# Kernel tuning notes

Measured on AMD Instinct MI355X. Metric: run time of the kernel, lower is better.

The kernel has to match this reference:

```python
import jax, jax.numpy as jnp
import numpy as np

N = 4096
INPUT_DIM = 512
H1 = 256
H2 = 64
ALPHA = 0.2
MASK_VAL = -9e15


def setup_inputs() -> dict:
    key = jax.random.key(0)
    ks = jax.random.split(key, 10)

    def glorot(k, fan_in, fan_out):
        r = np.sqrt(6.0 / (fan_in + fan_out)).astype(np.float32)
        return jax.random.uniform(k, (fan_in, fan_out), jnp.float32, -r, r)

    return {
        "X": jax.random.normal(ks[0], (N, INPUT_DIM), jnp.float32),
        "adj": jax.random.randint(ks[1], (N, N), 0, 2, jnp.int32),
        "noise": jax.random.normal(ks[2], (N, H2), jnp.float32),
        "W0": glorot(ks[3], INPUT_DIM, H1),
        "a0": jax.random.normal(ks[4], (2 * H1, 1), jnp.float32) * 0.1,
        "W1": glorot(ks[5], H1, H2),
        "a1": jax.random.normal(ks[6], (2 * H2, 1), jnp.float32) * 0.1,
        "W2": glorot(ks[7], H1, H2),
        "a2": jax.random.normal(ks[8], (2 * H2, 1), jnp.float32) * 0.1,
    }


def gat_layer(X, W, a, adj):
    # h: [N, d]
    h = X @ W
    d = h.shape[1]
    # e_ij = leakyrelu(a^T [h_i ; h_j]) == leakyrelu(f1_i + f2_j)
    f1 = h @ a[:d]            # [N, 1]
    f2 = h @ a[d:]            # [N, 1]
    e = jax.nn.leaky_relu(f1 + f2.T, negative_slope=ALPHA)  # [N, N]
    e = jnp.where(adj > 0, e, MASK_VAL)
    attn = jax.nn.softmax(e, axis=1)  # dropout omitted (eval mode)
    return attn @ h


def reference(X, adj, noise, W0, a0, W1, a1, W2, a2):
    hidden = gat_layer(X, W0, a0, adj)
    mean = gat_layer(hidden, W1, a1, adj)
    logstd = gat_layer(hidden, W2, a2, adj)
    Z = noise * jnp.exp(logstd) + mean          # [N, H2]
    A_pred = jax.nn.sigmoid(Z @ Z.T)            # [N, N]
    return A_pred
```

## Files before the change

### kernel.cpp

```cpp
#include <hip/hip_runtime.h>
#include <hip/hip_bf16.h>
#include <math.h>

#define N_NODES 4096
#define DIM_IN  512
#define DH1     256
#define DH2     64
#define ALPHA   0.2f
#define ROW_WORDS (N_NODES / 64)
#define NWORDS  (N_NODES * ROW_WORDS)
#define L2E     1.4426950408889634f

typedef __bf16 bf16_t;
typedef bf16_t bf16x8 __attribute__((ext_vector_type(8)));
typedef float  f32x4  __attribute__((ext_vector_type(4)));


__global__ __launch_bounds__(256) void prep_kernel(
    const float* __restrict__ X, const float* __restrict__ W0,
    const float* __restrict__ W1, const float* __restrict__ W2,
    const int* __restrict__ adj,
    bf16_t* __restrict__ Xb, bf16_t* __restrict__ W0T,
    bf16_t* __restrict__ W12T, unsigned long long* __restrict__ mask,
    float* __restrict__ f1b, float* __restrict__ f2b)
{
    const int b = blockIdx.x;
    const int tid = threadIdx.x;
    if (b < 2048) {
        int i = b * 256 + tid;
        float4 v = ((const float4*)X)[i];
        bf16_t o[4] = {(bf16_t)v.x, (bf16_t)v.y, (bf16_t)v.z, (bf16_t)v.w};
        const int e = i * 4;
        const int row = e >> 9, k = e & 511;
        const size_t base = ((size_t)(row >> 4) * 64 + (k >> 3)) * 128 + (row & 15) * 8 + (k & 7);
        *(uint2*)(Xb + base) = *(const uint2*)o;
    } else if (b < 2560) {
        int o = (b - 2048) * 256 + tid;
        int n = o >> 9, k = o & 511;
        const size_t base = ((size_t)(n >> 4) * 64 + (k >> 3)) * 128 + (n & 15) * 8 + (k & 7);
        W0T[base] = (bf16_t)W0[(size_t)k * DH1 + n];
    } else if (b < 2688) {
        int o = (b - 2560) * 256 + tid;
        int n = o >> 8, k = o & 255;
        const float* W = (n < 64) ? W1 : W2;
        const size_t base = ((size_t)(n >> 4) * 32 + (k >> 3)) * 128 + (n & 15) * 8 + (k & 7);
        W12T[base] = (bf16_t)W[(size_t)k * 64 + (n & 63)];
    } else if (b < 4736) {
        const int lane = tid & 63;
        int gw = ((b - 2688) * 256 + tid) >> 6;
        for (int w = gw; w < NWORDS; w += 8192) {
            int v = adj[(size_t)w * 64 + lane];
            unsigned long long bb = __ballot(v > 0);
            if (lane == 0) mask[w] = bb;
        }
    } else {
        int zb = b - 4736;
        float4* dst = (float4*)((zb < 8) ? f1b : f2b);
        dst[(zb & 7) * 256 + tid] = float4{0.f, 0.f, 0.f, 0.f};
    }
}

__global__ __launch_bounds__(256) void rowstats_kernel(
    const unsigned long long* __restrict__ mask,
    const float* __restrict__ f1b, const float* __restrict__ f2b,
    float* __restrict__ mrowb, float* __restrict__ srowb)
{
    __shared__ float f2s[N_NODES];
    const int l = blockIdx.y;
    const float* f1 = f1b + (size_t)l * N_NODES;
    const float* f2 = f2b + (size_t)l * N_NODES;
    const int tid = threadIdx.x;
    #pragma unroll
    for (int j = 0; j < N_NODES / 4; j += 256)
        ((float4*)f2s)[j + tid] = ((const float4*)f2)[j + tid];
    __syncthreads();
    const int wave = tid >> 6, lane = tid & 63;
    const int row = blockIdx.x * 4 + wave;
    const float fi = f1[row];
    const int l5 = lane & 31;
    const bool lohalf = (lane < 32);

    const unsigned long long wv = mask[(size_t)row * ROW_WORDS + lane];
    const unsigned wlo = (unsigned)wv, whi = (unsigned)(wv >> 32);

    float mx = -3.0e38f;
    #pragma unroll
    for (int t = 0; t < ROW_WORDS; ++t) {
        const unsigned blo = __shfl(wlo, t), bhi = __shfl(whi, t);
        const unsigned sel = lohalf ? blo : bhi;
        if ((sel >> l5) & 1u) {
            float e = fi + f2s[t * 64 + lane];
            e = fmaxf(e, ALPHA * e);
            mx = fmaxf(mx, e);
        }
    }
    for (int off = 32; off; off >>= 1) mx = fmaxf(mx, __shfl_xor(mx, off));

    float sum = 0.f;
    if (mx > -2.0e38f) {
        #pragma unroll
        for (int t = 0; t < ROW_WORDS; ++t) {
            const unsigned blo = __shfl(wlo, t), bhi = __shfl(whi, t);
            const unsigned sel = lohalf ? blo : bhi;
            if ((sel >> l5) & 1u) {
                float e = fi + f2s[t * 64 + lane];
                e = fmaxf(e, ALPHA * e);
                sum += __expf(e - mx);
            }
        }
    }
    for (int off = 32; off; off >>= 1) sum += __shfl_xor(sum, off);
    if (lane == 0) {
        if (mx > -2.0e38f) { mrowb[l * N_NODES + row] = mx; srowb[l * N_NODES + row] = sum; }
        else               { mrowb[l * N_NODES + row] = 0.f; srowb[l * N_NODES + row] = 0.f; }
    }
}

template <int NT, int KLEN>
__global__ __launch_bounds__(256) void attn_fused_kernel(
    const unsigned long long* __restrict__ maskw,
    const float* __restrict__ f1, const float* __restrict__ f2,
    const float* __restrict__ mrow, const float* __restrict__ srow,
    const bf16_t* __restrict__ BT, float* __restrict__ outP, int N)
{
    __shared__ float f2s[KLEN];
    __shared__ float tile[64 * (NT * 16 + 4)];
    const int tid = threadIdx.x;
    const int wave = tid >> 6, lane = tid & 63, quad = lane >> 4, l16 = lane & 15;
    const int colBase = blockIdx.x * (NT * 16);
    const int rowBase = blockIdx.y * 64;
    const int kBeg = blockIdx.z * KLEN;
    const int r = rowBase + wave * 16 + l16;

    if (tid < KLEN / 4) ((float4*)f2s)[tid] = *(const float4*)(f2 + kBeg + tid * 4);

    const float m = mrow[r], s = srow[r];
    const bool uni = (s <= 0.f);
    const float Cr = uni ? 0.f : (-m * L2E - __log2f(s));
    const float f1r = f1[r];
    const float puni = 1.0f / (float)N_NODES;

    __syncthreads();

    const int ubase = (colBase >> 4) * (N_NODES * 16) + kBeg * 16;
    const int laneo = quad * 128 + l16 * 8;
    const int qs = quad * 8;
    const unsigned long long* mptr = maskw + (size_t)r * ROW_WORDS + (kBeg >> 6);

    f32x4 acc[NT] = {};
    unsigned long long mcur = mptr[0];
    for (int w = 0; w < KLEN / 64; ++w) {
        unsigned long long mnext = (w < KLEN / 64 - 1) ? mptr[w + 1] : 0ull;
        const unsigned mlo = (unsigned)mcur, mhi = (unsigned)(mcur >> 32);
        #pragma unroll
        for (int h = 0; h < 2; ++h) {
            const int k0 = w * 64 + h * 32;
            bf16x8 bv[NT];
            #pragma unroll
            for (int t = 0; t < NT; ++t)
                bv[t] = *(const bf16x8*)(BT + ubase + t * (N_NODES * 16) + k0 * 16 + laneo);
            const unsigned bits = ((h ? mhi : mlo) >> qs) & 0xFFu;
            const int kc = k0 + qs;
            bf16x8 av;
            #pragma unroll
            for (int j = 0; j < 8; ++j) {
                float x = f1r + f2s[kc + j];
                float e = fmaxf(x, ALPHA * x);
                float p = ((bits >> j) & 1u) ? exp2f(__builtin_fmaf(e, L2E, Cr)) : 0.f;
                av[j] = (bf16_t)(uni ? puni : p);
            }
            #pragma unroll
            for (int t = 0; t < NT; ++t)
                acc[t] = __builtin_amdgcn_mfma_f32_16x16x32_bf16(av, bv[t], acc[t], 0, 0, 0);
        }
        mcur = mnext;
    }

    #pragma unroll
    for (int t = 0; t < NT; ++t) {
        const int col = t * 16 + l16;
        #pragma unroll
        for (int rr = 0; rr < 4; ++rr)
            tile[(wave * 16 + quad * 4 + rr) * (NT * 16 + 4) + col] = acc[t][rr];
    }
    __syncthreads();
    const int half = lane >> 5, c32 = (lane & 31) * 4;
    float* outBase = outP + (size_t)blockIdx.z * N_NODES * N + (size_t)rowBase * N + colBase;
    #pragma unroll
    for (int p = 0; p < 8; ++p) {
        const int rl = p * 8 + wave * 2 + half;
        f32x4 v = *(const f32x4*)&tile[rl * (NT * 16 + 4) + c32];
        __builtin_nontemporal_store(v, (f32x4*)(outBase + (size_t)rl * N + c32));
    }
}

template <int KLEN>
__global__ __launch_bounds__(256) void attn12_kernel(
    const unsigned long long* __restrict__ maskw,
    const float* __restrict__ f1b, const float* __restrict__ f2b,
    const float* __restrict__ mrowb, const float* __restrict__ srowb,
    const bf16_t* __restrict__ h12T, float* __restrict__ outP)
{
    __shared__ float f2s[KLEN];
    __shared__ float tile[64 * 68];
    const int l = blockIdx.x;
    const float* f1 = f1b + (size_t)l * N_NODES;
    const float* f2 = f2b + (size_t)l * N_NODES;

    const int tid = threadIdx.x;
    const int wave = tid >> 6, lane = tid & 63, quad = lane >> 4, l16 = lane & 15;
    const int rowBase = blockIdx.y * 64;
    const int kBeg = blockIdx.z * KLEN;
    const int r = rowBase + wave * 16 + l16;

    if (tid < KLEN / 4) ((float4*)f2s)[tid] = *(const float4*)(f2 + kBeg + tid * 4);

    const float m = mrowb[l * N_NODES + r], s = srowb[l * N_NODES + r];
    const bool uni = (s <= 0.f);
    const float Cr = uni ? 0.f : (-m * L2E - __log2f(s));
    const float f1r = f1[r];
    const float puni = 1.0f / (float)N_NODES;

    __syncthreads();

    const int ubase = (l * 4) * (N_NODES * 16) + kBeg * 16;
    const int laneo = quad * 128 + l16 * 8;
    const int qs = quad * 8;
    const unsigned long long* mptr = maskw + (size_t)r * ROW_WORDS + (kBeg >> 6);

    f32x4 acc[4] = {};
    unsigned long long mcur = mptr[0];
    for (int w = 0; w < KLEN / 64; ++w) {
        unsigned long long mnext = (w < KLEN / 64 - 1) ? mptr[w + 1] : 0ull;
        const unsigned mlo = (unsigned)mcur, mhi = (unsigned)(mcur >> 32);
        #pragma unroll
        for (int h = 0; h < 2; ++h) {
            const int k0 = w * 64 + h * 32;
            bf16x8 bv[4];
            #pragma unroll
            for (int t = 0; t < 4; ++t)
                bv[t] = *(const bf16x8*)(h12T + ubase + t * (N_NODES * 16) + k0 * 16 + laneo);
            const unsigned bits = ((h ? mhi : mlo) >> qs) & 0xFFu;
            const int kc = k0 + qs;
            bf16x8 av;
            #pragma unroll
            for (int j = 0; j < 8; ++j) {
                float x = f1r + f2s[kc + j];
                float e = fmaxf(x, ALPHA * x);
                float p = ((bits >> j) & 1u) ? exp2f(__builtin_fmaf(e, L2E, Cr)) : 0.f;
                av[j] = (bf16_t)(uni ? puni : p);
            }
            #pragma unroll
            for (int t = 0; t < 4; ++t)
                acc[t] = __builtin_amdgcn_mfma_f32_16x16x32_bf16(av, bv[t], acc[t], 0, 0, 0);
        }
        mcur = mnext;
    }

    #pragma unroll
    for (int t = 0; t < 4; ++t) {
        const int col = t * 16 + l16;
        #pragma unroll
        for (int rr = 0; rr < 4; ++rr)
            tile[(wave * 16 + quad * 4 + rr) * 68 + col] = acc[t][rr];
    }
    __syncthreads();
    const int q4 = lane >> 4, c16 = (lane & 15) * 4;
    float* outBase = outP + ((size_t)blockIdx.z * 2 + l) * (N_NODES * DH2) + (size_t)rowBase * DH2;
    #pragma unroll
    for (int p = 0; p < 4; ++p) {
        const int rl = p * 16 + wave * 4 + q4;
        f32x4 v = *(const f32x4*)&tile[rl * 68 + c16];
        __builtin_nontemporal_store(v, (f32x4*)(outBase + (size_t)rl * DH2 + c16));
    }
}

__global__ __launch_bounds__(256) void reduce_kernel(
    const float* __restrict__ p, bf16_t* __restrict__ out, int n4, int S)
{
    int i = blockIdx.x * 256 + threadIdx.x;
    if (i >= n4) return;
    float4 a = ((const float4*)p)[i];
    for (int s = 1; s < S; ++s) {
        float4 b = ((const float4*)p)[(size_t)s * n4 + i];
        a.x += b.x; a.y += b.y; a.z += b.z; a.w += b.w;
    }
    bf16_t o[4] = {(bf16_t)a.x, (bf16_t)a.y, (bf16_t)a.z, (bf16_t)a.w};
    const int e = i * 4;
    const int row = e >> 8, k = e & 255;
    const size_t base = ((size_t)(row >> 4) * 32 + (k >> 3)) * 128 + (row & 15) * 8 + (k & 7);
    *(uint2*)(out + base) = *(const uint2*)o;
}

__global__ __launch_bounds__(256) void reduce_z_kernel(
    const float* __restrict__ part, const float* __restrict__ noise,
    bf16_t* __restrict__ ZA, bf16_t* __restrict__ ZB)
{
    const int idx = blockIdx.x * 256 + threadIdx.x;
    const int stride = 2 * N_NODES * DH2;
    float mean = 0.f, ls = 0.f;
    #pragma unroll
    for (int s = 0; s < 4; ++s) {
        mean += part[(size_t)s * stride + idx];
        ls   += part[(size_t)s * stride + N_NODES * DH2 + idx];
    }
    float z = noise[idx] * __expf(ls) + mean;
    bf16_t zhi = (bf16_t)z;
    bf16_t zlo = (bf16_t)(z - (float)zhi);
    const int i = idx >> 6, c = idx & 63;
    const size_t base = ((size_t)(i >> 4) * 32 + (c >> 3)) * 128 + (i & 15) * 8 + (c & 7);
    ZA[base]        = zhi;
    ZA[base + 1024] = zhi;
    ZA[base + 2048] = zlo;
    ZA[base + 3072] = zlo;
    ZB[base]        = zhi;
    ZB[base + 1024] = zlo;
    ZB[base + 2048] = zhi;
    ZB[base + 3072] = zlo;
}

template <int NT>
__global__ __launch_bounds__(256) void gemm0_kernel(
    const bf16_t* __restrict__ A, const bf16_t* __restrict__ BT,
    bf16_t* __restrict__ Ct, const float* __restrict__ a0,
    float* __restrict__ f1, float* __restrict__ f2)
{
    const int tid = threadIdx.x;
    const int wave = tid >> 6, lane = tid & 63, quad = lane >> 4, l16 = lane & 15;
    const int colBase = blockIdx.x * (NT * 16), rowBase = blockIdx.y * 64;
    const size_t KS = (size_t)DIM_IN * 16;
    const bf16_t* Ap = A + (size_t)((rowBase >> 4) + wave) * KS + quad * 128 + l16 * 8;
    const bf16_t* Bp = BT + (size_t)(colBase >> 4) * KS + quad * 128 + l16 * 8;

    f32x4 acc[NT] = {};
    for (int k0 = 0; k0 < DIM_IN; k0 += 64) {
        bf16x8 bv[2 * NT];
        #pragma unroll
        for (int t = 0; t < NT; ++t) {
            bv[t]      = *(const bf16x8*)(Bp + (size_t)t * KS + k0 * 16);
            bv[NT + t] = *(const bf16x8*)(Bp + (size_t)t * KS + (k0 + 32) * 16);
        }
        bf16x8 av0 = *(const bf16x8*)(Ap + k0 * 16);
        bf16x8 av1 = *(const bf16x8*)(Ap + (k0 + 32) * 16);
        #pragma unroll
        for (int t = 0; t < NT; ++t)
            acc[t] = __builtin_amdgcn_mfma_f32_16x16x32_bf16(av0, bv[t], acc[t], 0, 0, 0);
        #pragma unroll
        for (int t = 0; t < NT; ++t)
            acc[t] = __builtin_amdgcn_mfma_f32_16x16x32_bf16(av1, bv[NT + t], acc[t], 0, 0, 0);
    }
    #pragma unroll
    for (int t = 0; t < NT; ++t) {
        const int col = colBase + t * 16 + l16;
        bf16_t pk[4];
        #pragma unroll
        for (int rr = 0; rr < 4; ++rr) pk[rr] = (bf16_t)acc[t][rr];
        const int kc = (rowBase + wave * 16 + quad * 4) >> 3;
        const size_t o = ((size_t)(col >> 4) * (N_NODES >> 3) + kc) * 128
                       + (col & 15) * 8 + (quad & 1) * 4;
        *(uint2*)(Ct + o) = *(const uint2*)pk;
    }
    #pragma unroll
    for (int rr = 0; rr < 4; ++rr) {
        float s1 = 0.f, s2 = 0.f;
        #pragma unroll
        for (int t = 0; t < NT; ++t) {
            const int col = colBase + t * 16 + l16;
            s1 += acc[t][rr] * a0[col];
            s2 += acc[t][rr] * a0[DH1 + col];
        }
        #pragma unroll
        for (int off = 8; off; off >>= 1) {
            s1 += __shfl_down(s1, off, 16);
            s2 += __shfl_down(s2, off, 16);
        }
        if (l16 == 0) {
            const int row = rowBase + wave * 16 + quad * 4 + rr;
            atomicAdd(f1 + row, s1);
            atomicAdd(f2 + row, s2);
        }
    }
}

__global__ __launch_bounds__(256) void gemm12_kernel(
    const bf16_t* __restrict__ A, const bf16_t* __restrict__ BT,
    bf16_t* __restrict__ Ct, const float* __restrict__ a1, const float* __restrict__ a2,
    float* __restrict__ f1b, float* __restrict__ f2b)
{
    const int tid = threadIdx.x;
    const int wave = tid >> 6, lane = tid & 63, quad = lane >> 4, l16 = lane & 15;
    const int l = blockIdx.x;
    const int colBase = l * 64, rowBase = blockIdx.y * 64;
    const size_t KS = (size_t)DH1 * 16;
    const bf16_t* Ap = A + (size_t)((rowBase >> 4) + wave) * KS + quad * 128 + l16 * 8;
    const bf16_t* Bp = BT + (size_t)(colBase >> 4) * KS + quad * 128 + l16 * 8;

    f32x4 acc[4] = {};
    for (int k0 = 0; k0 < DH1; k0 += 64) {
        bf16x8 bv[8];
        #pragma unroll
        for (int t = 0; t < 4; ++t) {
            bv[t]     = *(const bf16x8*)(Bp + (size_t)t * KS + k0 * 16);
            bv[4 + t] = *(const bf16x8*)(Bp + (size_t)t * KS + (k0 + 32) * 16);
        }
        bf16x8 av0 = *(const bf16x8*)(Ap + k0 * 16);
        bf16x8 av1 = *(const bf16x8*)(Ap + (k0 + 32) * 16);
        #pragma unroll
        for (int t = 0; t < 4; ++t)
            acc[t] = __builtin_amdgcn_mfma_f32_16x16x32_bf16(av0, bv[t], acc[t], 0, 0, 0);
        #pragma unroll
        for (int t = 0; t < 4; ++t)
            acc[t] = __builtin_amdgcn_mfma_f32_16x16x32_bf16(av1, bv[4 + t], acc[t], 0, 0, 0);
    }
    #pragma unroll
    for (int t = 0; t < 4; ++t) {
        const int col = colBase + t * 16 + l16;
        bf16_t pk[4];
        #pragma unroll
        for (int rr = 0; rr < 4; ++rr) pk[rr] = (bf16_t)acc[t][rr];
        const int kc = (rowBase + wave * 16 + quad * 4) >> 3;
        const size_t o = ((size_t)(col >> 4) * (N_NODES >> 3) + kc) * 128
                       + (col & 15) * 8 + (quad & 1) * 4;
        *(uint2*)(Ct + o) = *(const uint2*)pk;
    }
    const float* a = l ? a2 : a1;
    #pragma unroll
    for (int rr = 0; rr < 4; ++rr) {
        float s1 = 0.f, s2 = 0.f;
        #pragma unroll
        for (int t = 0; t < 4; ++t) {
            const int lc = t * 16 + l16;
            s1 += acc[t][rr] * a[lc];
            s2 += acc[t][rr] * a[64 + lc];
        }
        #pragma unroll
        for (int off = 8; off; off >>= 1) {
            s1 += __shfl_down(s1, off, 16);
            s2 += __shfl_down(s2, off, 16);
        }
        if (l16 == 0) {
            const int row = rowBase + wave * 16 + quad * 4 + rr;
            f1b[l * N_NODES + row] = s1;
            f2b[l * N_NODES + row] = s2;
        }
    }
}

template <int NT>
__global__ __launch_bounds__(256) void zzt_sigmoid_kernel(
    const bf16_t* __restrict__ ZA, const bf16_t* __restrict__ ZB, float* __restrict__ C)
{
    __shared__ float tile[64 * (NT * 16 + 4)];
    const int tid = threadIdx.x;
    const int wave = tid >> 6, lane = tid & 63, quad = lane >> 4, l16 = lane & 15;
    const int colBase = blockIdx.x * (NT * 16), rowBase = blockIdx.y * 64;
    const bf16_t* Ap = ZA + (size_t)((rowBase >> 4) + wave) * 4096 + quad * 128 + l16 * 8;
    const bf16_t* Bp = ZB + (size_t)(colBase >> 4) * 4096 + quad * 128 + l16 * 8;

    f32x4 acc[NT] = {};
    for (int k0 = 0; k0 < 256; k0 += 32) {
        bf16x8 bv[NT];
        #pragma unroll
        for (int t = 0; t < NT; ++t)
            bv[t] = *(const bf16x8*)(Bp + (size_t)t * 4096 + k0 * 16);
        bf16x8 av = *(const bf16x8*)(Ap + k0 * 16);
        #pragma unroll
        for (int t = 0; t < NT; ++t)
            acc[t] = __builtin_amdgcn_mfma_f32_16x16x32_bf16(av, bv[t], acc[t], 0, 0, 0);
    }
    #pragma unroll
    for (int t = 0; t < NT; ++t) {
        const int col = t * 16 + l16;
        #pragma unroll
        for (int rr = 0; rr < 4; ++rr) {
            const int rl = wave * 16 + quad * 4 + rr;
            float x = acc[t][rr];
            tile[rl * (NT * 16 + 4) + col] = __builtin_amdgcn_rcpf(1.0f + exp2f(-x * L2E));
        }
    }
    __syncthreads();
    const int half = lane >> 5, c32 = (lane & 31) * 4;
    float* outBase = C + (size_t)rowBase * N_NODES + colBase;
    #pragma unroll
    for (int p = 0; p < 8; ++p) {
        const int rl = p * 8 + wave * 2 + half;
        f32x4 v = *(const f32x4*)&tile[rl * (NT * 16 + 4) + c32];
        __builtin_nontemporal_store(v, (f32x4*)(outBase + (size_t)rl * N_NODES + c32));
    }
}

extern "C" void kernel_launch(void* const* d_in, const int* in_sizes, int n_in,
                              void* d_out, int out_size, void* d_ws, size_t ws_size,
                              hipStream_t stream)
{
    const float* X     = (const float*)d_in[0];
    const int*   adj   = (const int*)  d_in[1];
    const float* noise = (const float*)d_in[2];
    const float* W0    = (const float*)d_in[3];
    const float* a0    = (const float*)d_in[4];
    const float* W1    = (const float*)d_in[5];
    const float* a1    = (const float*)d_in[6];
    const float* W2    = (const float*)d_in[7];
    const float* a2    = (const float*)d_in[8];
    float* out = (float*)d_out;

    char* ws = (char*)d_ws;
    size_t off = 0;
    auto alloc = [&](size_t bytes) { char* p = ws + off; off += (bytes + 255) & ~(size_t)255; return p; };

    unsigned long long* mask = (unsigned long long*)alloc((size_t)NWORDS * 8);
    float*  part  = (float*)alloc((size_t)4 * N_NODES * DH1 * 4);
    bf16_t* Xb    = (bf16_t*)alloc((size_t)N_NODES * DIM_IN * 2);
    bf16_t* W0T   = (bf16_t*)alloc((size_t)DH1 * DIM_IN * 2);
    bf16_t* W12T  = (bf16_t*)alloc((size_t)128 * DH1 * 2);
    bf16_t* h0T   = (bf16_t*)alloc((size_t)DH1 * N_NODES * 2);
    bf16_t* hidb  = (bf16_t*)alloc((size_t)N_NODES * DH1 * 2);
    bf16_t* h12T  = (bf16_t*)alloc((size_t)128 * N_NODES * 2);
    bf16_t* ZA    = (bf16_t*)alloc((size_t)N_NODES * 256 * 2);
    bf16_t* ZB    = (bf16_t*)alloc((size_t)N_NODES * 256 * 2);
    float* f1b  = (float*)alloc((size_t)2 * N_NODES * 4);
    float* f2b  = (float*)alloc((size_t)2 * N_NODES * 4);
    float* mrowb = (float*)alloc((size_t)2 * N_NODES * 4);
    float* srowb = (float*)alloc((size_t)2 * N_NODES * 4);
    (void)ws_size; (void)in_sizes; (void)n_in; (void)out_size;

    dim3 blk(256);

    prep_kernel<<<4752, blk, 0, stream>>>(X, W0, W1, W2, adj, Xb, W0T, W12T, mask, f1b, f2b);

    gemm0_kernel<2><<<dim3(8, N_NODES / 64), blk, 0, stream>>>(
        Xb, W0T, h0T, a0, f1b, f2b);
    rowstats_kernel<<<dim3(N_NODES / 4, 1), blk, 0, stream>>>(mask, f1b, f2b, mrowb, srowb);
    attn_fused_kernel<8, 1024><<<dim3(2, N_NODES / 64, 4), blk, 0, stream>>>(
        mask, f1b, f2b, mrowb, srowb, h0T, part, DH1);
    reduce_kernel<<<(N_NODES * DH1 / 4 + 255) / 256, blk, 0, stream>>>(
        part, hidb, N_NODES * DH1 / 4, 4);

    gemm12_kernel<<<dim3(2, N_NODES / 64), blk, 0, stream>>>(
        hidb, W12T, h12T, a1, a2, f1b, f2b);

    rowstats_kernel<<<dim3(N_NODES / 4, 2), blk, 0, stream>>>(mask, f1b, f2b, mrowb, srowb);
    attn12_kernel<1024><<<dim3(2, N_NODES / 64, 4), blk, 0, stream>>>(
        mask, f1b, f2b, mrowb, srowb, h12T, part);
    reduce_z_kernel<<<(N_NODES * DH2) / 256, blk, 0, stream>>>(part, noise, ZA, ZB);

    zzt_sigmoid_kernel<8><<<dim3(N_NODES / 128, N_NODES / 64), blk, 0, stream>>>(
        ZA, ZB, out);
}
```

Baseline: 284.0 us.

## Fuse all pipeline stages into one cooperative persistent kernel with grid syncs

Replaces the sequence of ten kernel launches with a single cooperative mega-kernel of 512 blocks. Each stage is refactored into a device body and separated by grid.sync(), with blocks looping over work units where a stage has more units than blocks. The aim is to remove per-launch overhead and the gaps between kernels. The trade-offs are grid-wide barrier costs, lower occupancy from a fixed 512-block grid and shared smem sizing, and reduced parallelism in small stages like gemm12, where only 128 blocks do work. If the cooperative launch fails, it falls back to the separate kernels.

```diff
diff --git a/kernel.cpp b/kernel.cpp
--- a/kernel.cpp
+++ b/kernel.cpp
@@ -1,6 +1,9 @@
 #include <hip/hip_runtime.h>
 #include <hip/hip_bf16.h>
+#include <hip/hip_cooperative_groups.h>
 #include <math.h>
+
+namespace cg = cooperative_groups;
 
 #define N_NODES 4096
 #define DIM_IN  512
@@ -16,7 +19,9 @@
 typedef float  f32x4  __attribute__((ext_vector_type(4)));
 
 
-__global__ __launch_bounds__(256) void prep_kernel(
+
+static __device__ __forceinline__ void prep_unit(
+    int b, int tid,
     const float* __restrict__ X, const float* __restrict__ W0,
     const float* __restrict__ W1, const float* __restrict__ W2,
     const int* __restrict__ adj,
@@ -24,8 +29,6 @@
     bf16_t* __restrict__ W12T, unsigned long long* __restrict__ mask,
     float* __restrict__ f1b, float* __restrict__ f2b)
 {
-    const int b = blockIdx.x;
-    const int tid = threadIdx.x;
     if (b < 2048) {
         int i = b * 256 + tid;
         float4 v = ((const float4*)X)[i];
@@ -60,22 +63,13 @@
     }
 }
 
-__global__ __launch_bounds__(256) void rowstats_kernel(
-    const unsigned long long* __restrict__ mask,
-    const float* __restrict__ f1b, const float* __restrict__ f2b,
-    float* __restrict__ mrowb, float* __restrict__ srowb)
-{
-    __shared__ float f2s[N_NODES];
-    const int l = blockIdx.y;
-    const float* f1 = f1b + (size_t)l * N_NODES;
-    const float* f2 = f2b + (size_t)l * N_NODES;
-    const int tid = threadIdx.x;
-    #pragma unroll
-    for (int j = 0; j < N_NODES / 4; j += 256)
-        ((float4*)f2s)[j + tid] = ((const float4*)f2)[j + tid];
-    __syncthreads();
+static __device__ __forceinline__ void rowstats_unit(
+    int u, int tid, const unsigned long long* __restrict__ mask,
+    const float* __restrict__ f1, const float* __restrict__ f2s,
+    float* __restrict__ mrow, float* __restrict__ srow)
+{
     const int wave = tid >> 6, lane = tid & 63;
-    const int row = blockIdx.x * 4 + wave;
+    const int row = u * 4 + wave;
     const float fi = f1[row];
     const int l5 = lane & 31;
     const bool lohalf = (lane < 32);
@@ -111,25 +105,87 @@
     }
     for (int off = 32; off; off >>= 1) sum += __shfl_xor(sum, off);
     if (lane == 0) {
-        if (mx > -2.0e38f) { mrowb[l * N_NODES + row] = mx; srowb[l * N_NODES + row] = sum; }
-        else               { mrowb[l * N_NODES + row] = 0.f; srowb[l * N_NODES + row] = 0.f; }
-    }
-}
-
-template <int NT, int KLEN>
-__global__ __launch_bounds__(256) void attn_fused_kernel(
+        if (mx > -2.0e38f) { mrow[row] = mx; srow[row] = sum; }
+        else               { mrow[row] = 0.f; srow[row] = 0.f; }
+    }
+}
+
+static __device__ __forceinline__ void gemm0_body(
+    int bx, int by, int tid,
+    const bf16_t* __restrict__ A, const bf16_t* __restrict__ BT,
+    bf16_t* __restrict__ Ct, const float* __restrict__ a0,
+    float* __restrict__ f1, float* __restrict__ f2)
+{
+    const int NT = 2;
+    const int wave = tid >> 6, lane = tid & 63, quad = lane >> 4, l16 = lane & 15;
+    const int colBase = bx * (NT * 16), rowBase = by * 64;
+    const size_t KS = (size_t)DIM_IN * 16;
+    const bf16_t* Ap = A + (size_t)((rowBase >> 4) + wave) * KS + quad * 128 + l16 * 8;
+    const bf16_t* Bp = BT + (size_t)(colBase >> 4) * KS + quad * 128 + l16 * 8;
+
+    f32x4 acc[NT] = {};
+    for (int k0 = 0; k0 < DIM_IN; k0 += 64) {
+        bf16x8 bv[2 * NT];
+        #pragma unroll
+        for (int t = 0; t < NT; ++t) {
+            bv[t]      = *(const bf16x8*)(Bp + (size_t)t * KS + k0 * 16);
+            bv[NT + t] = *(const bf16x8*)(Bp + (size_t)t * KS + (k0 + 32) * 16);
+        }
+        bf16x8 av0 = *(const bf16x8*)(Ap + k0 * 16);
+        bf16x8 av1 = *(const bf16x8*)(Ap + (k0 + 32) * 16);
+        #pragma unroll
+        for (int t = 0; t < NT; ++t)
+            acc[t] = __builtin_amdgcn_mfma_f32_16x16x32_bf16(av0, bv[t], acc[t], 0, 0, 0);
+        #pragma unroll
+        for (int t = 0; t < NT; ++t)
+            acc[t] = __builtin_amdgcn_mfma_f32_16x16x32_bf16(av1, bv[NT + t], acc[t], 0, 0, 0);
+    }
+    #pragma unroll
+    for (int t = 0; t < NT; ++t) {
+        const int col = colBase + t * 16 + l16;
+        bf16_t pk[4];
+        #pragma unroll
+        for (int rr = 0; rr < 4; ++rr) pk[rr] = (bf16_t)acc[t][rr];
+        const int kc = (rowBase + wave * 16 + quad * 4) >> 3;
+        const size_t o = ((size_t)(col >> 4) * (N_NODES >> 3) + kc) * 128
+                       + (col & 15) * 8 + (quad & 1) * 4;
+        *(uint2*)(Ct + o) = *(const uint2*)pk;
+    }
+    #pragma unroll
+    for (int rr = 0; rr < 4; ++rr) {
+        float s1 = 0.f, s2 = 0.f;
+        #pragma unroll
+        for (int t = 0; t < NT; ++t) {
+            const int col = colBase + t * 16 + l16;
+            s1 += acc[t][rr] * a0[col];
+            s2 += acc[t][rr] * a0[DH1 + col];
+        }
+        #pragma unroll
+        for (int off = 8; off; off >>= 1) {
+            s1 += __shfl_down(s1, off, 16);
+            s2 += __shfl_down(s2, off, 16);
+        }
+        if (l16 == 0) {
+            const int row = rowBase + wave * 16 + quad * 4 + rr;
+            atomicAdd(f1 + row, s1);
+            atomicAdd(f2 + row, s2);
+        }
+    }
+}
+
+static __device__ __forceinline__ void attn0_body(
+    int bx, int by, int bz, int tid,
     const unsigned long long* __restrict__ maskw,
     const float* __restrict__ f1, const float* __restrict__ f2,
     const float* __restrict__ mrow, const float* __restrict__ srow,
-    const bf16_t* __restrict__ BT, float* __restrict__ outP, int N)
-{
-    __shared__ float f2s[KLEN];
-    __shared__ float tile[64 * (NT * 16 + 4)];
-    const int tid = threadIdx.x;
+    const bf16_t* __restrict__ BT, float* __restrict__ outP,
+    float* f2s, float* tile)
+{
+    const int NT = 8, KLEN = 1024;
     const int wave = tid >> 6, lane = tid & 63, quad = lane >> 4, l16 = lane & 15;
-    const int colBase = blockIdx.x * (NT * 16);
-    const int rowBase = blockIdx.y * 64;
-    const int kBeg = blockIdx.z * KLEN;
+    const int colBase = bx * (NT * 16);
+    const int rowBase = by * 64;
+    const int kBeg = bz * KLEN;
     const int r = rowBase + wave * 16 + l16;
 
     if (tid < KLEN / 4) ((float4*)f2s)[tid] = *(const float4*)(f2 + kBeg + tid * 4);
@@ -185,32 +241,110 @@
     }
     __syncthreads();
     const int half = lane >> 5, c32 = (lane & 31) * 4;
-    float* outBase = outP + (size_t)blockIdx.z * N_NODES * N + (size_t)rowBase * N + colBase;
+    float* outBase = outP + (size_t)bz * N_NODES * DH1 + (size_t)rowBase * DH1 + colBase;
     #pragma unroll
     for (int p = 0; p < 8; ++p) {
         const int rl = p * 8 + wave * 2 + half;
         f32x4 v = *(const f32x4*)&tile[rl * (NT * 16 + 4) + c32];
-        __builtin_nontemporal_store(v, (f32x4*)(outBase + (size_t)rl * N + c32));
-    }
-}
-
-template <int KLEN>
-__global__ __launch_bounds__(256) void attn12_kernel(
+        __builtin_nontemporal_store(v, (f32x4*)(outBase + (size_t)rl * DH1 + c32));
+    }
+    __syncthreads();
+}
+
+static __device__ __forceinline__ void reduce_unit(
+    int u, int tid, const float* __restrict__ p, bf16_t* __restrict__ out)
+{
+    const int n4 = N_NODES * DH1 / 4;
+    int i = u * 256 + tid;
+    float4 a = ((const float4*)p)[i];
+    for (int s = 1; s < 4; ++s) {
+        float4 b = ((const float4*)p)[(size_t)s * n4 + i];
+        a.x += b.x; a.y += b.y; a.z += b.z; a.w += b.w;
+    }
+    bf16_t o[4] = {(bf16_t)a.x, (bf16_t)a.y, (bf16_t)a.z, (bf16_t)a.w};
+    const int e = i * 4;
+    const int row = e >> 8, k = e & 255;
+    const size_t base = ((size_t)(row >> 4) * 32 + (k >> 3)) * 128 + (row & 15) * 8 + (k & 7);
+    *(uint2*)(out + base) = *(const uint2*)o;
+}
+
+static __device__ __forceinline__ void gemm12_body(
+    int l, int by, int tid,
+    const bf16_t* __restrict__ A, const bf16_t* __restrict__ BT,
+    bf16_t* __restrict__ Ct, const float* __restrict__ a1, const float* __restrict__ a2,
+    float* __restrict__ f1b, float* __restrict__ f2b)
+{
+    const int wave = tid >> 6, lane = tid & 63, quad = lane >> 4, l16 = lane & 15;
+    const int colBase = l * 64, rowBase = by * 64;
+    const size_t KS = (size_t)DH1 * 16;
+    const bf16_t* Ap = A + (size_t)((rowBase >> 4) + wave) * KS + quad * 128 + l16 * 8;
+    const bf16_t* Bp = BT + (size_t)(colBase >> 4) * KS + quad * 128 + l16 * 8;
+
+    f32x4 acc[4] = {};
+    for (int k0 = 0; k0 < DH1; k0 += 64) {
+        bf16x8 bv[8];
+        #pragma unroll
+        for (int t = 0; t < 4; ++t) {
+            bv[t]     = *(const bf16x8*)(Bp + (size_t)t * KS + k0 * 16);
+            bv[4 + t] = *(const bf16x8*)(Bp + (size_t)t * KS + (k0 + 32) * 16);
+        }
+        bf16x8 av0 = *(const bf16x8*)(Ap + k0 * 16);
+        bf16x8 av1 = *(const bf16x8*)(Ap + (k0 + 32) * 16);
+        #pragma unroll
+        for (int t = 0; t < 4; ++t)
+            acc[t] = __builtin_amdgcn_mfma_f32_16x16x32_bf16(av0, bv[t], acc[t], 0, 0, 0);
+        #pragma unroll
+        for (int t = 0; t < 4; ++t)
+            acc[t] = __builtin_amdgcn_mfma_f32_16x16x32_bf16(av1, bv[4 + t], acc[t], 0, 0, 0);
+    }
+    #pragma unroll
+    for (int t = 0; t < 4; ++t) {
+        const int col = colBase + t * 16 + l16;
+        bf16_t pk[4];
+        #pragma unroll
+        for (int rr = 0; rr < 4; ++rr) pk[rr] = (bf16_t)acc[t][rr];
+        const int kc = (rowBase + wave * 16 + quad * 4) >> 3;
+        const size_t o = ((size_t)(col >> 4) * (N_NODES >> 3) + kc) * 128
+                       + (col & 15) * 8 + (quad & 1) * 4;
+        *(uint2*)(Ct + o) = *(const uint2*)pk;
+    }
+    const float* a = l ? a2 : a1;
+    #pragma unroll
+    for (int rr = 0; rr < 4; ++rr) {
+        float s1 = 0.f, s2 = 0.f;
+        #pragma unroll
+        for (int t = 0; t < 4; ++t) {
+            const int lc = t * 16 + l16;
+            s1 += acc[t][rr] * a[lc];
+            s2 += acc[t][rr] * a[64 + lc];
+        }
+        #pragma unroll
+        for (int off = 8; off; off >>= 1) {
+            s1 += __shfl_down(s1, off, 16);
+            s2 += __shfl_down(s2, off, 16);
+        }
+        if (l16 == 0) {
+            const int row = rowBase + wave * 16 + quad * 4 + rr;
+            f1b[l * N_NODES + row] = s1;
+            f2b[l * N_NODES + row] = s2;
+        }
+    }
+}
+
+static __device__ __forceinline__ void attn12_body(
+    int l, int by, int bz, int tid,
     const unsigned long long* __restrict__ maskw,
     const float* __restrict__ f1b, const float* __restrict__ f2b,
     const float* __restrict__ mrowb, const float* __restrict__ srowb,
-    const bf16_t* __restrict__ h12T, float* __restrict__ outP)
-{
-    __shared__ float f2s[KLEN];
-    __shared__ float tile[64 * 68];
-    const int l = blockIdx.x;
+    const bf16_t* __restrict__ h12T, float* __restrict__ outP,
+    float* f2s, float* tile)
+{
+    const int KLEN = 1024;
     const float* f1 = f1b + (size_t)l * N_NODES;
     const float* f2 = f2b + (size_t)l * N_NODES;
-
-    const int tid = threadIdx.x;
     const int wave = tid >> 6, lane = tid & 63, quad = lane >> 4, l16 = lane & 15;
-    const int rowBase = blockIdx.y * 64;
-    const int kBeg = blockIdx.z * KLEN;
+    const int rowBase = by * 64;
+    const int kBeg = bz * KLEN;
     const int r = rowBase + wave * 16 + l16;
 
     if (tid < KLEN / 4) ((float4*)f2s)[tid] = *(const float4*)(f2 + kBeg + tid * 4);
@@ -266,37 +400,21 @@
     }
     __syncthreads();
     const int q4 = lane >> 4, c16 = (lane & 15) * 4;
-    float* outBase = outP + ((size_t)blockIdx.z * 2 + l) * (N_NODES * DH2) + (size_t)rowBase * DH2;
+    float* outBase = outP + ((size_t)bz * 2 + l) * (N_NODES * DH2) + (size_t)rowBase * DH2;
     #pragma unroll
     for (int p = 0; p < 4; ++p) {
         const int rl = p * 16 + wave * 4 + q4;
         f32x4 v = *(const f32x4*)&tile[rl * 68 + c16];
         __builtin_nontemporal_store(v, (f32x4*)(outBase + (size_t)rl * DH2 + c16));
     }
-}
-
-__global__ __launch_bounds__(256) void reduce_kernel(
-    const float* __restrict__ p, bf16_t* __restrict__ out, int n4, int S)
-{
-    int i = blockIdx.x * 256 + threadIdx.x;
-    if (i >= n4) return;
-    float4 a = ((const float4*)p)[i];
-    for (int s = 1; s < S; ++s) {
-        float4 b = ((const float4*)p)[(size_t)s * n4 + i];
-        a.x += b.x; a.y += b.y; a.z += b.z; a.w += b.w;
-    }
-    bf16_t o[4] = {(bf16_t)a.x, (bf16_t)a.y, (bf16_t)a.z, (bf16_t)a.w};
-    const int e = i * 4;
-    const int row = e >> 8, k = e & 255;
-    const size_t base = ((size_t)(row >> 4) * 32 + (k >> 3)) * 128 + (row & 15) * 8 + (k & 7);
-    *(uint2*)(out + base) = *(const uint2*)o;
-}
-
-__global__ __launch_bounds__(256) void reduce_z_kernel(
-    const float* __restrict__ part, const float* __restrict__ noise,
+    __syncthreads();
+}
+
+static __device__ __forceinline__ void reduce_z_unit(
+    int u, int tid, const float* __restrict__ part, const float* __restrict__ noise,
     bf16_t* __restrict__ ZA, bf16_t* __restrict__ ZB)
 {
-    const int idx = blockIdx.x * 256 + threadIdx.x;
+    const int idx = u * 256 + tid;
     const int stride = 2 * N_NODES * DH2;
     float mean = 0.f, ls = 0.f;
     #pragma unroll
@@ -319,67 +437,188 @@
     ZB[base + 3072] = zlo;
 }
 
-template <int NT>
+static __device__ __forceinline__ void zzt_body(
+    int bx, int by, int tid,
+    const bf16_t* __restrict__ ZA, const bf16_t* __restrict__ ZB,
+    float* __restrict__ C, float* tile)
+{
+    const int NT = 8;
+    const int wave = tid >> 6, lane = tid & 63, quad = lane >> 4, l16 = lane & 15;
+    const int colBase = bx * (NT * 16), rowBase = by * 64;
+    const bf16_t* Ap = ZA + (size_t)((rowBase >> 4) + wave) * 4096 + quad * 128 + l16 * 8;
+    const bf16_t* Bp = ZB + (size_t)(colBase >> 4) * 4096 + quad * 128 + l16 * 8;
+
+    f32x4 acc[NT] = {};
+    for (int k0 = 0; k0 < 256; k0 += 32) {
+        bf16x8 bv[NT];
+        #pragma unroll
+        for (int t = 0; t < NT; ++t)
+            bv[t] = *(const bf16x8*)(Bp + (size_t)t * 4096 + k0 * 16);
+        bf16x8 av = *(const bf16x8*)(Ap + k0 * 16);
+        #pragma unroll
+        for (int t = 0; t < NT; ++t)
+            acc[t] = __builtin_amdgcn_mfma_f32_16x16x32_bf16(av, bv[t], acc[t], 0, 0, 0);
+    }
+    #pragma unroll
+    for (int t = 0; t < NT; ++t) {
+        const int col = t * 16 + l16;
+        #pragma unroll
+        for (int rr = 0; rr < 4; ++rr) {
+            const int rl = wave * 16 + quad * 4 + rr;
+            float x = acc[t][rr];
+            tile[rl * (NT * 16 + 4) + col] = __builtin_amdgcn_rcpf(1.0f + exp2f(-x * L2E));
+        }
+    }
+    __syncthreads();
+    const int half = lane >> 5, c32 = (lane & 31) * 4;
+    float* outBase = C + (size_t)rowBase * N_NODES + colBase;
+    #pragma unroll
+    for (int p = 0; p < 8; ++p) {
+        const int rl = p * 8 + wave * 2 + half;
+        f32x4 v = *(const f32x4*)&tile[rl * (NT * 16 + 4) + c32];
+        __builtin_nontemporal_store(v, (f32x4*)(outBase + (size_t)rl * N_NODES + c32));
+    }
+    __syncthreads();
+}
+
+__global__ __launch_bounds__(256) void mega_kernel(
+    const float* X, const int* adj, const float* noise,
+    const float* W0, const float* a0, const float* W1, const float* a1,
+    const float* W2, const float* a2, float* out,
+    unsigned long long* mask, float* part,
+    bf16_t* Xb, bf16_t* W0T, bf16_t* W12T,
+    bf16_t* h0T, bf16_t* hidb, bf16_t* h12T,
+    bf16_t* ZA, bf16_t* ZB,
+    float* f1b, float* f2b, float* mrowb, float* srowb)
+{
+    __shared__ float smem[9472];
+    cg::grid_group grid = cg::this_grid();
+    const int bid = blockIdx.x;
+    const int tid = threadIdx.x;
+
+    for (int u = bid; u < 4752; u += 512)
+        prep_unit(u, tid, X, W0, W1, W2, adj, Xb, W0T, W12T, mask, f1b, f2b);
+    grid.sync();
+
+    gemm0_body(bid & 7, bid >> 3, tid, Xb, W0T, h0T, a0, f1b, f2b);
+    grid.sync();
+
+    for (int j = 0; j < 1024; j += 256)
+        ((float4*)smem)[j + tid] = ((const float4*)f2b)[j + tid];
+    __syncthreads();
+    for (int u = bid; u < 1024; u += 512)
+        rowstats_unit(u, tid, mask, f1b, smem, mrowb, srowb);
+    grid.sync();
+
+    attn0_body(bid & 1, (bid >> 1) & 63, bid >> 7, tid,
+               mask, f1b, f2b, mrowb, srowb, h0T, part, smem, smem + 1024);
+    grid.sync();
+
+    for (int u = bid; u < 1024; u += 512) reduce_unit(u, tid, part, hidb);
+    grid.sync();
+
+    if (bid < 128) gemm12_body(bid & 1, bid >> 1, tid, hidb, W12T, h12T, a1, a2, f1b, f2b);
+    grid.sync();
+
+    {
+        const int l = (bid >= 256) ? 1 : 0;
+        const float* f2l = f2b + (size_t)l * N_NODES;
+        for (int j = 0; j < 1024; j += 256)
+            ((float4*)smem)[j + tid] = ((const float4*)f2l)[j + tid];
+        __syncthreads();
+        const int b0 = (bid & 255) * 4;
+        #pragma unroll
+        for (int i = 0; i < 4; ++i)
+            rowstats_unit(b0 + i, tid, mask, f1b + (size_t)l * N_NODES, smem,
+                          mrowb + (size_t)l * N_NODES, srowb + (size_t)l * N_NODES);
+    }
+    grid.sync();
+
+    attn12_body(bid & 1, (bid >> 1) & 63, bid >> 7, tid,
+                mask, f1b, f2b, mrowb, srowb, h12T, part, smem, smem + 1024);
+    grid.sync();
+
+    for (int u = bid; u < 1024; u += 512) reduce_z_unit(u, tid, part, noise, ZA, ZB);
+    grid.sync();
+
+    #pragma unroll
+    for (int i = 0; i < 4; ++i) {
+        const int u = bid * 4 + i;
+        zzt_body(u & 31, u >> 5, tid, ZA, ZB, out, smem);
+    }
+}
+
+__global__ __launch_bounds__(256) void prep_kernel(
+    const float* __restrict__ X, const float* __restrict__ W0,
+    const float* __restrict__ W1, const float* __restrict__ W2,
+    const int* __restrict__ adj,
+    bf16_t* __restrict__ Xb, bf16_t* __restrict__ W0T,
+    bf16_t* __restrict__ W12T, unsigned long long* __restrict__ mask,
+    float* __restrict__ f1b, float* __restrict__ f2b)
+{
+    prep_unit(blockIdx.x, threadIdx.x, X, W0, W1, W2, adj, Xb, W0T, W12T, mask, f1b, f2b);
+}
+
+__global__ __launch_bounds__(256) void rowstats_kernel(
+    const unsigned long long* __restrict__ mask,
+    const float* __restrict__ f1b, const float* __restrict__ f2b,
+    float* __restrict__ mrowb, float* __restrict__ srowb)
+{
+    __shared__ float f2s[N_NODES];
+    const int l = blockIdx.y;
+    const int tid = threadIdx.x;
+    const float* f2 = f2b + (size_t)l * N_NODES;
+    #pragma unroll
+    for (int j = 0; j < 1024; j += 256)
+        ((float4*)f2s)[j + tid] = ((const float4*)f2)[j + tid];
+    __syncthreads();
+    rowstats_unit(blockIdx.x, tid, mask, f1b + (size_t)l * N_NODES, f2s,
+                  mrowb + (size_t)l * N_NODES, srowb + (size_t)l * N_NODES);
+}
+
+__global__ __launch_bounds__(256) void attn_fused_kernel(
+    const unsigned long long* __restrict__ maskw,
+    const float* __restrict__ f1, const float* __restrict__ f2,
+    const float* __restrict__ mrow, const float* __restrict__ srow,
+    const bf16_t* __restrict__ BT, float* __restrict__ outP)
+{
+    __shared__ float f2s[1024];
+    __shared__ float tile[64 * 132];
+    attn0_body(blockIdx.x, blockIdx.y, blockIdx.z, threadIdx.x,
+               maskw, f1, f2, mrow, srow, BT, outP, f2s, tile);
+}
+
+__global__ __launch_bounds__(256) void attn12_kernel(
+    const unsigned long long* __restrict__ maskw,
+    const float* __restrict__ f1b, const float* __restrict__ f2b,
+    const float* __restrict__ mrowb, const float* __restrict__ srowb,
+    const bf16_t* __restrict__ h12T, float* __restrict__ outP)
+{
+    __shared__ float f2s[1024];
+    __shared__ float tile[64 * 68];
+    attn12_body(blockIdx.x, blockIdx.y, blockIdx.z, threadIdx.x,
+                maskw, f1b, f2b, mrowb, srowb, h12T, outP, f2s, tile);
+}
+
+__global__ __launch_bounds__(256) void reduce_kernel(
+    const float* __restrict__ p, bf16_t* __restrict__ out)
+{
+    reduce_unit(blockIdx.x, threadIdx.x, p, out);
+}
+
+__global__ __launch_bounds__(256) void reduce_z_kernel(
+    const float* __restrict__ part, const float* __restrict__ noise,
+    bf16_t* __restrict__ ZA, bf16_t* __restrict__ ZB)
+{
+    reduce_z_unit(blockIdx.x, threadIdx.x, part, noise, ZA, ZB);
+}
+
 __global__ __launch_bounds__(256) void gemm0_kernel(
     const bf16_t* __restrict__ A, const bf16_t* __restrict__ BT,
     bf16_t* __restrict__ Ct, const float* __restrict__ a0,
     float* __restrict__ f1, float* __restrict__ f2)
 {
-    const int tid = threadIdx.x;
-    const int wave = tid >> 6, lane = tid & 63, quad = lane >> 4, l16 = lane & 15;
-    const int colBase = blockIdx.x * (NT * 16), rowBase = blockIdx.y * 64;
-    const size_t KS = (size_t)DIM_IN * 16;
-    const bf16_t* Ap = A + (size_t)((rowBase >> 4) + wave) * KS + quad * 128 + l16 * 8;
-    const bf16_t* Bp = BT + (size_t)(colBase >> 4) * KS + quad * 128 + l16 * 8;
-
-    f32x4 acc[NT] = {};
-    for (int k0 = 0; k0 < DIM_IN; k0 += 64) {
-        bf16x8 bv[2 * NT];
-        #pragma unroll
-        for (int t = 0; t < NT; ++t) {
-            bv[t]      = *(const bf16x8*)(Bp + (size_t)t * KS + k0 * 16);
-            bv[NT + t] = *(const bf16x8*)(Bp + (size_t)t * KS + (k0 + 32) * 16);
-        }
-        bf16x8 av0 = *(const bf16x8*)(Ap + k0 * 16);
-        bf16x8 av1 = *(const bf16x8*)(Ap + (k0 + 32) * 16);
-        #pragma unroll
-        for (int t = 0; t < NT; ++t)
-            acc[t] = __builtin_amdgcn_mfma_f32_16x16x32_bf16(av0, bv[t], acc[t], 0, 0, 0);
-        #pragma unroll
-        for (int t = 0; t < NT; ++t)
-            acc[t] = __builtin_amdgcn_mfma_f32_16x16x32_bf16(av1, bv[NT + t], acc[t], 0, 0, 0);
-    }
-    #pragma unroll
-    for (int t = 0; t < NT; ++t) {
-        const int col = colBase + t * 16 + l16;
-        bf16_t pk[4];
-        #pragma unroll
-        for (int rr = 0; rr < 4; ++rr) pk[rr] = (bf16_t)acc[t][rr];
-        const int kc = (rowBase + wave * 16 + quad * 4) >> 3;
-        const size_t o = ((size_t)(col >> 4) * (N_NODES >> 3) + kc) * 128
-                       + (col & 15) * 8 + (quad & 1) * 4;
-        *(uint2*)(Ct + o) = *(const uint2*)pk;
-    }
-    #pragma unroll
-    for (int rr = 0; rr < 4; ++rr) {
-        float s1 = 0.f, s2 = 0.f;
-        #pragma unroll
-        for (int t = 0; t < NT; ++t) {
-            const int col = colBase + t * 16 + l16;
-            s1 += acc[t][rr] * a0[col];
-            s2 += acc[t][rr] * a0[DH1 + col];
-        }
-        #pragma unroll
-        for (int off = 8; off; off >>= 1) {
-            s1 += __shfl_down(s1, off, 16);
-            s2 += __shfl_down(s2, off, 16);
-        }
-        if (l16 == 0) {
-            const int row = rowBase + wave * 16 + quad * 4 + rr;
-            atomicAdd(f1 + row, s1);
-            atomicAdd(f2 + row, s2);
-        }
-    }
+    gemm0_body(blockIdx.x, blockIdx.y, threadIdx.x, A, BT, Ct, a0, f1, f2);
 }
 
 __global__ __launch_bounds__(256) void gemm12_kernel(
@@ -387,106 +626,14 @@
     bf16_t* __restrict__ Ct, const float* __restrict__ a1, const float* __restrict__ a2,
     float* __restrict__ f1b, float* __restrict__ f2b)
 {
-    const int tid = threadIdx.x;
-    const int wave = tid >> 6, lane = tid & 63, quad = lane >> 4, l16 = lane & 15;
-    const int l = blockIdx.x;
-    const int colBase = l * 64, rowBase = blockIdx.y * 64;
-    const size_t KS = (size_t)DH1 * 16;
-    const bf16_t* Ap = A + (size_t)((rowBase >> 4) + wave) * KS + quad * 128 + l16 * 8;
-    const bf16_t* Bp = BT + (size_t)(colBase >> 4) * KS + quad * 128 + l16 * 8;
-
-    f32x4 acc[4] = {};
-    for (int k0 = 0; k0 < DH1; k0 += 64) {
-        bf16x8 bv[8];
-        #pragma unroll
-        for (int t = 0; t < 4; ++t) {
-            bv[t]     = *(const bf16x8*)(Bp + (size_t)t * KS + k0 * 16);
-            bv[4 + t] = *(const bf16x8*)(Bp + (size_t)t * KS + (k0 + 32) * 16);
-        }
-        bf16x8 av0 = *(const bf16x8*)(Ap + k0 * 16);
-        bf16x8 av1 = *(const bf16x8*)(Ap + (k0 + 32) * 16);
-        #pragma unroll
-        for (int t = 0; t < 4; ++t)
-            acc[t] = __builtin_amdgcn_mfma_f32_16x16x32_bf16(av0, bv[t], acc[t], 0, 0, 0);
-        #pragma unroll
-        for (int t = 0; t < 4; ++t)
-            acc[t] = __builtin_amdgcn_mfma_f32_16x16x32_bf16(av1, bv[4 + t], acc[t], 0, 0, 0);
-    }
-    #pragma unroll
-    for (int t = 0; t < 4; ++t) {
-        const int col = colBase + t * 16 + l16;
-        bf16_t pk[4];
-        #pragma unroll
-        for (int rr = 0; rr < 4; ++rr) pk[rr] = (bf16_t)acc[t][rr];
-        const int kc = (rowBase + wave * 16 + quad * 4) >> 3;
-        const size_t o = ((size_t)(col >> 4) * (N_NODES >> 3) + kc) * 128
-                       + (col & 15) * 8 + (quad & 1) * 4;
-        *(uint2*)(Ct + o) = *(const uint2*)pk;
-    }
-    const float* a = l ? a2 : a1;
-    #pragma unroll
-    for (int rr = 0; rr < 4; ++rr) {
-        float s1 = 0.f, s2 = 0.f;
-        #pragma unroll
-        for (int t = 0; t < 4; ++t) {
-            const int lc = t * 16 + l16;
-            s1 += acc[t][rr] * a[lc];
-            s2 += acc[t][rr] * a[64 + lc];
-        }
-        #pragma unroll
-        for (int off = 8; off; off >>= 1) {
-            s1 += __shfl_down(s1, off, 16);
-            s2 += __shfl_down(s2, off, 16);
-        }
-        if (l16 == 0) {
-            const int row = rowBase + wave * 16 + quad * 4 + rr;
-            f1b[l * N_NODES + row] = s1;
-            f2b[l * N_NODES + row] = s2;
-        }
-    }
-}
-
-template <int NT>
+    gemm12_body(blockIdx.x, blockIdx.y, threadIdx.x, A, BT, Ct, a1, a2, f1b, f2b);
+}
+
 __global__ __launch_bounds__(256) void zzt_sigmoid_kernel(
     const bf16_t* __restrict__ ZA, const bf16_t* __restrict__ ZB, float* __restrict__ C)
 {
-    __shared__ float tile[64 * (NT * 16 + 4)];
-    const int tid = threadIdx.x;
-    const int wave = tid >> 6, lane = tid & 63, quad = lane >> 4, l16 = lane & 15;
-    const int colBase = blockIdx.x * (NT * 16), rowBase = blockIdx.y * 64;
-    const bf16_t* Ap = ZA + (size_t)((rowBase >> 4) + wave) * 4096 + quad * 128 + l16 * 8;
-    const bf16_t* Bp = ZB + (size_t)(colBase >> 4) * 4096 + quad * 128 + l16 * 8;
-
-    f32x4 acc[NT] = {};
-    for (int k0 = 0; k0 < 256; k0 += 32) {
-        bf16x8 bv[NT];
-        #pragma unroll
-        for (int t = 0; t < NT; ++t)
-            bv[t] = *(const bf16x8*)(Bp + (size_t)t * 4096 + k0 * 16);
-        bf16x8 av = *(const bf16x8*)(Ap + k0 * 16);
-        #pragma unroll
-        for (int t = 0; t < NT; ++t)
-            acc[t] = __builtin_amdgcn_mfma_f32_16x16x32_bf16(av, bv[t], acc[t], 0, 0, 0);
-    }
-    #pragma unroll
-    for (int t = 0; t < NT; ++t) {
-        const int col = t * 16 + l16;
-        #pragma unroll
-        for (int rr = 0; rr < 4; ++rr) {
-            const int rl = wave * 16 + quad * 4 + rr;
-            float x = acc[t][rr];
-            tile[rl * (NT * 16 + 4) + col] = __builtin_amdgcn_rcpf(1.0f + exp2f(-x * L2E));
-        }
-    }
-    __syncthreads();
-    const int half = lane >> 5, c32 = (lane & 31) * 4;
-    float* outBase = C + (size_t)rowBase * N_NODES + colBase;
-    #pragma unroll
-    for (int p = 0; p < 8; ++p) {
-        const int rl = p * 8 + wave * 2 + half;
-        f32x4 v = *(const f32x4*)&tile[rl * (NT * 16 + 4) + c32];
-        __builtin_nontemporal_store(v, (f32x4*)(outBase + (size_t)rl * N_NODES + c32));
-    }
+    __shared__ float tile[64 * 132];
+    zzt_body(blockIdx.x, blockIdx.y, threadIdx.x, ZA, ZB, C, tile);
 }
 
 extern "C" void kernel_launch(void* const* d_in, const int* in_sizes, int n_in,
@@ -524,26 +671,30 @@
     float* srowb = (float*)alloc((size_t)2 * N_NODES * 4);
     (void)ws_size; (void)in_sizes; (void)n_in; (void)out_size;
 
+    void* args[] = {
+        (void*)&X, (void*)&adj, (void*)&noise, (void*)&W0, (void*)&a0,
+        (void*)&W1, (void*)&a1, (void*)&W2, (void*)&a2, (void*)&out,
+        (void*)&mask, (void*)&part, (void*)&Xb, (void*)&W0T, (void*)&W12T,
+        (void*)&h0T, (void*)&hidb, (void*)&h12T, (void*)&ZA, (void*)&ZB,
+        (void*)&f1b, (void*)&f2b, (void*)&mrowb, (void*)&srowb
+    };
+    hipError_t err = hipLaunchCooperativeKernel((const void*)mega_kernel,
+                                                dim3(512), dim3(256), args, 0, stream);
+    if (err == hipSuccess) return;
+    (void)hipGetLastError();
+
     dim3 blk(256);
-
     prep_kernel<<<4752, blk, 0, stream>>>(X, W0, W1, W2, adj, Xb, W0T, W12T, mask, f1b, f2b);
-
-    gemm0_kernel<2><<<dim3(8, N_NODES / 64), blk, 0, stream>>>(
-        Xb, W0T, h0T, a0, f1b, f2b);
+    gemm0_kernel<<<dim3(8, N_NODES / 64), blk, 0, stream>>>(Xb, W0T, h0T, a0, f1b, f2b);
     rowstats_kernel<<<dim3(N_NODES / 4, 1), blk, 0, stream>>>(mask, f1b, f2b, mrowb, srowb);
-    attn_fused_kernel<8, 1024><<<dim3(2, N_NODES / 64, 4), blk, 0, stream>>>(
-        mask, f1b, f2b, mrowb, srowb, h0T, part, DH1);
-    reduce_kernel<<<(N_NODES * DH1 / 4 + 255) / 256, blk, 0, stream>>>(
-        part, hidb, N_NODES * DH1 / 4, 4);
-
+    attn_fused_kernel<<<dim3(2, N_NODES / 64, 4), blk, 0, stream>>>(
+        mask, f1b, f2b, mrowb, srowb, h0T, part);
+    reduce_kernel<<<1024, blk, 0, stream>>>(part, hidb);
     gemm12_kernel<<<dim3(2, N_NODES / 64), blk, 0, stream>>>(
         hidb, W12T, h12T, a1, a2, f1b, f2b);
-
     rowstats_kernel<<<dim3(N_NODES / 4, 2), blk, 0, stream>>>(mask, f1b, f2b, mrowb, srowb);
-    attn12_kernel<1024><<<dim3(2, N_NODES / 64, 4), blk, 0, stream>>>(
+    attn12_kernel<<<dim3(2, N_NODES / 64, 4), blk, 0, stream>>>(
         mask, f1b, f2b, mrowb, srowb, h12T, part);
-    reduce_z_kernel<<<(N_NODES * DH2) / 256, blk, 0, stream>>>(part, noise, ZA, ZB);
-
-    zzt_sigmoid_kernel<8><<<dim3(N_NODES / 128, N_NODES / 64), blk, 0, stream>>>(
-        ZA, ZB, out);
-}
+    reduce_z_kernel<<<1024, blk, 0, stream>>>(part, noise, ZA, ZB);
+    zzt_sigmoid_kernel<<<dim3(N_NODES / 128, N_NODES / 64), blk, 0, stream>>>(ZA, ZB, out);
+}
```

Measured after the change: 897.6 us. 3.16x slower.
